# Kernel optimization log

Measured on AMD Instinct MI355X. Metric: run time of the kernel, lower is better.

## Reference

```python
import jax, jax.numpy as jnp
import numpy as np

D = 64       # link_state_dim
RU = 256     # readout_units
N = 50000    # num_edges (total links)
E = 800000   # number of (main, neighbour) message pairs
K_PATHS = 8
T_STEPS = 3


def setup_inputs() -> dict:
    key = jax.random.key(0)
    ks = jax.random.split(key, 10)
    std = 0.1  # init_weight uses normal(std=0.1) for Linear/GRUCell weights
    return {
        'links_state': jax.random.normal(ks[0], (N, D), dtype=jnp.float32),
        'id_mainEdges': jax.random.randint(ks[1], (E,), 0, N),
        'id_neighbourEdges': jax.random.randint(ks[2], (E,), 0, N),
        'W_msg': std * jax.random.normal(ks[3], (D, 2 * D), dtype=jnp.float32),
        'b_msg': jnp.zeros((D,), jnp.float32),
        'W_ih': std * jax.random.normal(ks[4], (3 * D, D), dtype=jnp.float32),
        'W_hh': std * jax.random.normal(ks[5], (3 * D, D), dtype=jnp.float32),
        'b_ih': jnp.zeros((3 * D,), jnp.float32),
        'b_hh': jnp.zeros((3 * D,), jnp.float32),
        'Wr1': std * jax.random.normal(ks[6], (RU, D), dtype=jnp.float32),
        'br1': jnp.zeros((RU,), jnp.float32),
        'Wr2': std * jax.random.normal(ks[7], (RU, RU), dtype=jnp.float32),
        'br2': jnp.zeros((RU,), jnp.float32),
        'Wr3': std * jax.random.normal(ks[8], (1, RU), dtype=jnp.float32),
        'br3': jnp.zeros((1,), jnp.float32),
        'K': K_PATHS,
        'T': T_STEPS,
        'num_edges': N,
    }


def _gru_cell(x, h, W_ih, W_hh, b_ih, b_hh):
    gi = x @ W_ih.T + b_ih            # [N, 3D]
    gh = h @ W_hh.T + b_hh            # [N, 3D]
    i_r, i_z, i_n = jnp.split(gi, 3, axis=1)
    h_r, h_z, h_n = jnp.split(gh, 3, axis=1)
    r = jax.nn.sigmoid(i_r + h_r)
    z = jax.nn.sigmoid(i_z + h_z)
    n = jnp.tanh(i_n + r * h_n)
    return (1.0 - z) * n + z * h


def reference(links_state, id_mainEdges, id_neighbourEdges, W_msg, b_msg,
              W_ih, W_hh, b_ih, b_hh, Wr1, br1, Wr2, br2, Wr3, br3,
              K, T, num_edges):
    for _ in range(T):  # fixed small message-passing depth
        # gather + concat: [E, 2D]
        cat = jnp.concatenate([links_state[id_mainEdges],
                               links_state[id_neighbourEdges]], axis=1)
        m = jax.nn.selu(cat @ W_msg.T + b_msg)                       # [E, D]
        links_M = jax.ops.segment_sum(m, id_neighbourEdges,
                                      num_segments=num_edges)        # [N, D]
        links_state = _gru_cell(links_M, links_state, W_ih, W_hh, b_ih, b_hh)
    # group edges into K paths (contiguous blocks, per K_paths_ids construction)
    per_path = num_edges // K
    path_ids = jnp.arange(num_edges) // per_path
    k_path_outputs = jax.ops.segment_sum(links_state, path_ids,
                                         num_segments=K)             # [K, D]
    h = jax.nn.selu(k_path_outputs @ Wr1.T + br1)
    h = jax.nn.selu(h @ Wr2.T + br2)
    logits = (h @ Wr3.T + br3).reshape(-1)                           # [K]
    return jax.nn.softmax(logits)  # Categorical probs over K paths
```

## Files before the change

### kernel.cpp

```cpp
#include <hip/hip_runtime.h>
#include <hip/hip_bf16.h>

#define D 64
#define CAP 5120

typedef _Float16 f16;
typedef _Float16 f16x2 __attribute__((ext_vector_type(2)));
typedef _Float16 f16x4 __attribute__((ext_vector_type(4)));
typedef _Float16 f16x8 __attribute__((ext_vector_type(8)));
typedef float f32x16 __attribute__((ext_vector_type(16)));

#define MFMA_F16(a, b, c) __builtin_amdgcn_mfma_f32_32x32x16_f16(a, b, c, 0, 0, 0)

__device__ __forceinline__ float selu_f(float x) {
    const float SC = 1.0507009873554805f;
    const float AL = 1.6732632423543772f;
    return x > 0.f ? SC * x : SC * AL * (__expf(x) - 1.f);
}
__device__ __forceinline__ float sigmoid_f(float x) { return 1.f / (1.f + __expf(-x)); }
__device__ __forceinline__ float tanh_f(float x) {
    float s = x < 0.f ? -1.f : 1.f;
    float t = __expf(-2.f * fabsf(x));
    return s * (1.f - t) / (1.f + t);
}
__device__ __forceinline__ float dot4(float4 a, float4 b, float acc) {
    acc = fmaf(a.x, b.x, acc);
    acc = fmaf(a.y, b.y, acc);
    acc = fmaf(a.z, b.z, acc);
    return fmaf(a.w, b.w, acc);
}
__device__ __forceinline__ f32x16 zero16() {
    f32x16 v;
#pragma unroll
    for (int i = 0; i < 16; ++i) v[i] = 0.f;
    return v;
}

__global__ void __launch_bounds__(256) bucketpack_kernel(
    const int* __restrict__ idm, const int* __restrict__ idn,
    int* __restrict__ cursor, uint2* __restrict__ barr,
    const float* __restrict__ Wih, const float* __restrict__ Whh,
    const float* __restrict__ Wmsg, f16* __restrict__ w16,
    float* __restrict__ kp, int* __restrict__ rdcnt,
    int E, int NBK, int NBB) {
    __shared__ int hist[256];
    __shared__ int gbase[256];
    __shared__ int loff[256];
    int t = threadIdx.x;
    if ((int)blockIdx.x >= NBB) {
        int idx = ((int)blockIdx.x - NBB) * 256 + t;
        if (idx < 512) kp[idx] = 0.f;
        if (idx == 0) *rdcnt = 0;
        int g = idx >> 12;
        int rem = idx & 4095;
        int d = rem >> 6, k0 = rem & 63;
        float v;
        if (g < 3)      v = Wih[(g * 64 + d) * 64 + k0];
        else if (g < 6) v = Whh[((g - 3) * 64 + d) * 64 + k0];
        else            v = Wmsg[d * 128 + (g - 6) * 64 + k0];
        w16[g * 4096 + d * 64 + (k0 ^ ((d & 7) << 3))] = (f16)v;
        return;
    }
    if (t < NBK) hist[t] = 0;
    __syncthreads();
    int tile = blockIdx.x * 2048;
    int n_[8], m_[8], b_[8];
#pragma unroll
    for (int j = 0; j < 8; ++j) {
        int e = tile + j * 256 + t;
        if (e < E) {
            n_[j] = idn[e];
            m_[j] = idm[e];
            b_[j] = n_[j] >> 8;
            atomicAdd(&hist[b_[j]], 1);
        } else {
            b_[j] = -1;
        }
    }
    __syncthreads();
    if (t < NBK) {
        gbase[t] = hist[t] ? atomicAdd(&cursor[t], hist[t]) : 0;
        loff[t] = 0;
    }
    __syncthreads();
#pragma unroll
    for (int j = 0; j < 8; ++j) {
        if (b_[j] >= 0) {
            int r = atomicAdd(&loff[b_[j]], 1);
            uint2 e;
            e.x = (unsigned)n_[j];
            e.y = (unsigned)m_[j];
            barr[(size_t)b_[j] * CAP + gbase[b_[j]] + r] = e;
        }
    }
}

__global__ void __launch_bounds__(256) csryz0_kernel(
    const uint2* __restrict__ barr, const int* __restrict__ cursor,
    int* __restrict__ row_start, int* __restrict__ csr_src,
    const float* __restrict__ x, const f16* __restrict__ w16,
    f16* __restrict__ y16, f16* __restrict__ z16,
    int N, int E, int NT, int NBK, int YZGRID) {
    __shared__ int hist[256];
    __shared__ int offs[256];
    __shared__ int curc[256];
    __shared__ int red[256];
    __shared__ int ldsIdm[CAP];
    __shared__ int baseSh;
    __shared__ __align__(16) f16 wlds[2 * 4096];
    __shared__ __align__(16) f16 xh[64 * 64];
    int t = threadIdx.x;
    if ((int)blockIdx.x < NBK) {
        int b = blockIdx.x;
        int cntb = cursor[b];
        red[t] = (t < b) ? cursor[t] : 0;
        __syncthreads();
        for (int off = 128; off > 0; off >>= 1) {
            if (t < off) red[t] += red[t + off];
            __syncthreads();
        }
        if (t == 0) baseSh = red[0];
        hist[t] = 0;
        __syncthreads();
        int base = baseSh;
        for (int i = t; i < cntb; i += 256) {
            int n = (int)(barr[(size_t)b * CAP + i].x) & 255;
            atomicAdd(&hist[n], 1);
        }
        __syncthreads();
        int v0 = hist[t];
        offs[t] = v0;
        __syncthreads();
        for (int off = 1; off < 256; off <<= 1) {
            int v = offs[t];
            int u = (t >= off) ? offs[t - off] : 0;
            __syncthreads();
            offs[t] = v + u;
            __syncthreads();
        }
        int excl = offs[t] - v0;
        curc[t] = excl;
        int node = (b << 8) + t;
        if (node < N) row_start[node] = base + excl;
        if (b == NBK - 1 && t == 0) row_start[N] = E;
        __syncthreads();
        for (int i = t; i < cntb; i += 256) {
            uint2 e = barr[(size_t)b * CAP + i];
            int r = atomicAdd(&curc[e.x & 255], 1);
            ldsIdm[r] = (int)e.y;
        }
        __syncthreads();
        for (int i = t; i < cntb; i += 256) csr_src[base + i] = ldsIdm[i];
        return;
    }
    int yb = (int)blockIdx.x - NBK;
#pragma unroll
    for (int it = 0; it < 4; ++it) {
        int idx = (it * 256 + t) * 8;
        *(f16x8*)&wlds[idx] = *(const f16x8*)&w16[6 * 4096 + idx];
    }
    int lane = t & 63;
    int w = t >> 6;
    int ng = w >> 1;
    int dh = w & 1;
    int arow = ng * 32 + (lane & 31);
    int arow64 = arow * 64;
    int axor = (arow & 7) << 3;
    int bcol = dh * 32 + (lane & 31);
    int bxor = (bcol & 7) << 3;
    int kg = (lane >> 5) * 8;
    __syncthreads();
    for (int tile = yb; tile < NT; tile += YZGRID) {
        int base = tile * 64;
#pragma unroll
        for (int it = 0; it < 4; ++it) {
            int idx = it * 256 + t;
            int node = idx >> 4, k0 = (idx & 15) * 4;
            int gn = base + node;
            f16x4 v;
            if (gn < N) {
                float4 f4 = *(const float4*)&x[(size_t)gn * 64 + k0];
                v[0] = (f16)f4.x; v[1] = (f16)f4.y; v[2] = (f16)f4.z; v[3] = (f16)f4.w;
            } else {
#pragma unroll
                for (int u = 0; u < 4; ++u) v[u] = (f16)0.f;
            }
            *(f16x4*)&xh[node * 64 + (k0 ^ ((node & 7) << 3))] = v;
        }
        __syncthreads();
        f32x16 aY = zero16(), aZ = zero16();
#pragma unroll
        for (int ks = 0; ks < 4; ++ks) {
            int kb = ks * 16 + kg;
            f16x8 ah = *(const f16x8*)&xh[arow64 + (kb ^ axor)];
            int wof = bcol * 64 + (kb ^ bxor);
            aY = MFMA_F16(ah, *(const f16x8*)&wlds[0 * 4096 + wof], aY);
            aZ = MFMA_F16(ah, *(const f16x8*)&wlds[1 * 4096 + wof], aZ);
        }
#pragma unroll
        for (int r = 0; r < 16; ++r) {
            int rowC = (r & 3) + 8 * (r >> 2) + 4 * (lane >> 5);
            int gn = base + ng * 32 + rowC;
            if (gn < N) {
                size_t o = (size_t)gn * 64 + bcol;
                y16[o] = (f16)aY[r];
                z16[o] = (f16)aZ[r];
            }
        }
        __syncthreads();
    }
}

__global__ void __launch_bounds__(256) gather_kernel(
    const f16* __restrict__ y16, const f16* __restrict__ z16,
    const float* __restrict__ bmsg, const int* __restrict__ row_start,
    const int* __restrict__ csr_src, f16* __restrict__ M16, int N) {
    int lane = threadIdx.x & 63;
    int sub = lane >> 5;
    int d0 = (lane & 31) * 2;
    int wave = blockIdx.x * (blockDim.x >> 6) + (threadIdx.x >> 6);
    int nwaves = gridDim.x * (blockDim.x >> 6);
    float b0 = bmsg[d0], b1 = bmsg[d0 + 1];
    for (int i = wave; i < N; i += nwaves) {
        f16x2 zv = *(const f16x2*)&z16[(size_t)i * 64 + d0];
        float zb0 = (float)zv[0] + b0;
        float zb1 = (float)zv[1] + b1;
        int s1 = row_start[i + 1];
        float m0 = 0.f, m1 = 0.f;
        int s = row_start[i] + sub;
        for (; s + 6 < s1; s += 8) {
            int e0 = csr_src[s],     e1 = csr_src[s + 2];
            int e2 = csr_src[s + 4], e3 = csr_src[s + 6];
            f16x2 v0 = *(const f16x2*)&y16[(size_t)e0 * 64 + d0];
            f16x2 v1 = *(const f16x2*)&y16[(size_t)e1 * 64 + d0];
            f16x2 v2 = *(const f16x2*)&y16[(size_t)e2 * 64 + d0];
            f16x2 v3 = *(const f16x2*)&y16[(size_t)e3 * 64 + d0];
            m0 += selu_f((float)v0[0] + zb0);
            m1 += selu_f((float)v0[1] + zb1);
            m0 += selu_f((float)v1[0] + zb0);
            m1 += selu_f((float)v1[1] + zb1);
            m0 += selu_f((float)v2[0] + zb0);
            m1 += selu_f((float)v2[1] + zb1);
            m0 += selu_f((float)v3[0] + zb0);
            m1 += selu_f((float)v3[1] + zb1);
        }
        for (; s < s1; s += 2) {
            int e0 = csr_src[s];
            f16x2 v0 = *(const f16x2*)&y16[(size_t)e0 * 64 + d0];
            m0 += selu_f((float)v0[0] + zb0);
            m1 += selu_f((float)v0[1] + zb1);
        }
        m0 += __shfl_xor(m0, 32, 64);
        m1 += __shfl_xor(m1, 32, 64);
        if (sub == 0) {
            f16x2 mv; mv[0] = (f16)m0; mv[1] = (f16)m1;
            *(f16x2*)&M16[(size_t)i * 64 + d0] = mv;
        }
    }
}

__global__ void __launch_bounds__(256, 2) gruyz_kernel(
    const f16* __restrict__ M16, const float* __restrict__ hin,
    float* __restrict__ hout,
    const float* __restrict__ bih, const float* __restrict__ bhh,
    const f16* __restrict__ w16, f16* __restrict__ y16, f16* __restrict__ z16,
    float* __restrict__ kp, int N, int NT, int PER, int doYZ) {
    __shared__ __align__(16) f16 wlds[8 * 4096];
    __shared__ __align__(16) f16 xm[64 * 64];
    __shared__ __align__(16) f16 xh[64 * 64];
    int t = threadIdx.x;
#pragma unroll 4
    for (int it = 0; it < 16; ++it) {
        int idx = (it * 256 + t) * 8;
        *(f16x8*)&wlds[idx] = *(const f16x8*)&w16[idx];
    }
    int lane = t & 63;
    int w = t >> 6;
    int ng = w >> 1;
    int dh = w & 1;
    int arow = ng * 32 + (lane & 31);
    int arow64 = arow * 64;
    int axor = (arow & 7) << 3;
    int bcol = dh * 32 + (lane & 31);
    int bxor = (bcol & 7) << 3;
    int kg = (lane >> 5) * 8;
    float bIR = bih[bcol], bIZ = bih[64 + bcol], bIN = bih[128 + bcol];
    float bHR = bhh[bcol], bHZ = bhh[64 + bcol], bHN = bhh[128 + bcol];
    float* pathbuf = (float*)xm;
    __syncthreads();
    for (int tile = blockIdx.x; tile < NT; tile += gridDim.x) {
        int base = tile * 64;
#pragma unroll
        for (int it = 0; it < 2; ++it) {
            int idx = it * 256 + t;
            int node = idx >> 3, k0 = (idx & 7) * 8;
            int gn = base + node;
            f16x8 v;
            if (gn < N) v = *(const f16x8*)&M16[(size_t)gn * 64 + k0];
            else {
#pragma unroll
                for (int u = 0; u < 8; ++u) v[u] = (f16)0.f;
            }
            *(f16x8*)&xm[node * 64 + (k0 ^ ((node & 7) << 3))] = v;
        }
#pragma unroll
        for (int it = 0; it < 4; ++it) {
            int idx = it * 256 + t;
            int node = idx >> 4, k0 = (idx & 15) * 4;
            int gn = base + node;
            f16x4 v;
            if (gn < N) {
                float4 f4 = *(const float4*)&hin[(size_t)gn * 64 + k0];
                v[0] = (f16)f4.x; v[1] = (f16)f4.y; v[2] = (f16)f4.z; v[3] = (f16)f4.w;
            } else {
#pragma unroll
                for (int u = 0; u < 4; ++u) v[u] = (f16)0.f;
            }
            *(f16x4*)&xh[node * 64 + (k0 ^ ((node & 7) << 3))] = v;
        }
        __syncthreads();

        f32x16 aIR = zero16(), aIZ = zero16(), aIN = zero16();
        f32x16 aHR = zero16(), aHZ = zero16(), aHN = zero16();
#pragma unroll
        for (int ks = 0; ks < 4; ++ks) {
            int kb = ks * 16 + kg;
            f16x8 am = *(const f16x8*)&xm[arow64 + (kb ^ axor)];
            f16x8 ah = *(const f16x8*)&xh[arow64 + (kb ^ axor)];
            int wof = bcol * 64 + (kb ^ bxor);
            aIR = MFMA_F16(am, *(const f16x8*)&wlds[0 * 4096 + wof], aIR);
            aIZ = MFMA_F16(am, *(const f16x8*)&wlds[1 * 4096 + wof], aIZ);
            aIN = MFMA_F16(am, *(const f16x8*)&wlds[2 * 4096 + wof], aIN);
            aHR = MFMA_F16(ah, *(const f16x8*)&wlds[3 * 4096 + wof], aHR);
            aHZ = MFMA_F16(ah, *(const f16x8*)&wlds[4 * 4096 + wof], aHZ);
            aHN = MFMA_F16(ah, *(const f16x8*)&wlds[5 * 4096 + wof], aHN);
        }
        __syncthreads();

        int pbase = base / PER;
        int boundary = (pbase + 1) * PER;
        if (!doYZ) {
            if (t < 128) pathbuf[t] = 0.f;
            __syncthreads();
        }
#pragma unroll
        for (int r = 0; r < 16; ++r) {
            int rowC = (r & 3) + 8 * (r >> 2) + 4 * (lane >> 5);
            int nodeLocal = ng * 32 + rowC;
            int gn = base + nodeLocal;
            float hnew = 0.f;
            bool valid = gn < N;
            if (valid) {
                size_t o = (size_t)gn * 64 + bcol;
                float hold = hin[o];
                float rr = sigmoid_f(aIR[r] + bIR + aHR[r] + bHR);
                float zz = sigmoid_f(aIZ[r] + bIZ + aHZ[r] + bHZ);
                float nn = tanh_f(aIN[r] + bIN + rr * (aHN[r] + bHN));
                hnew = (1.f - zz) * nn + zz * hold;
                hout[o] = hnew;
            }
            if (doYZ) {
                xm[nodeLocal * 64 + (bcol ^ ((rowC & 7) << 3))] = (f16)hnew;
            } else if (valid) {
                int pidx = (gn >= boundary) ? 1 : 0;
                atomicAdd(&pathbuf[pidx * 64 + bcol], hnew);
            }
        }
        if (doYZ) {
            __syncthreads();
            f32x16 aY = zero16(), aZ = zero16();
#pragma unroll
            for (int ks = 0; ks < 4; ++ks) {
                int kb = ks * 16 + kg;
                f16x8 ahn2 = *(const f16x8*)&xm[arow64 + (kb ^ axor)];
                int wof = bcol * 64 + (kb ^ bxor);
                aY = MFMA_F16(ahn2, *(const f16x8*)&wlds[6 * 4096 + wof], aY);
                aZ = MFMA_F16(ahn2, *(const f16x8*)&wlds[7 * 4096 + wof], aZ);
            }
#pragma unroll
            for (int r = 0; r < 16; ++r) {
                int rowC = (r & 3) + 8 * (r >> 2) + 4 * (lane >> 5);
                int gn = base + ng * 32 + rowC;
                if (gn < N) {
                    size_t o = (size_t)gn * 64 + bcol;
                    y16[o] = (f16)aY[r];
                    z16[o] = (f16)aZ[r];
                }
            }
        } else {
            __syncthreads();
            if (t < 128) {
                int p = pbase + (t >> 6);
                float v = pathbuf[t];
                if (p < 8 && v != 0.f) atomicAdd(&kp[p * 64 + (t & 63)], v);
            }
        }
        __syncthreads();
    }
}

__global__ void __launch_bounds__(256) readout_kernel(
    const float* __restrict__ kp, const float* __restrict__ Wr1,
    const float* __restrict__ br1, const float* __restrict__ Wr2,
    const float* __restrict__ br2, const float* __restrict__ Wr3,
    const float* __restrict__ br3, float* __restrict__ lgbuf,
    int* __restrict__ rdcnt, float* __restrict__ out) {
    int p = blockIdx.x;
    int t = threadIdx.x;
    __shared__ __align__(16) float kps[64];
    __shared__ __align__(16) float h1[256];
    __shared__ float red[256];
    if (t < 64) kps[t] = kp[p * 64 + t];
    __syncthreads();
    float acc = br1[t];
#pragma unroll
    for (int d4 = 0; d4 < 16; ++d4) {
        float4 wv = *(const float4*)&Wr1[t * 64 + d4 * 4];
        float4 kv = *(const float4*)&kps[d4 * 4];
        acc = dot4(wv, kv, acc);
    }
    h1[t] = selu_f(acc);
    __syncthreads();
    float acc2 = br2[t];
#pragma unroll 8
    for (int j4 = 0; j4 < 64; ++j4) {
        float4 wv = *(const float4*)&Wr2[t * 256 + j4 * 4];
        float4 hv = *(const float4*)&h1[j4 * 4];
        acc2 = dot4(wv, hv, acc2);
    }
    float h2v = selu_f(acc2);
    red[t] = Wr3[t] * h2v;
    __syncthreads();
    for (int off = 128; off > 0; off >>= 1) {
        if (t < off) red[t] += red[t + off];
        __syncthreads();
    }
    if (t == 0) {
        float logit = red[0] + br3[0];
        atomicExch(&lgbuf[p], logit);
        __threadfence();
        int old = atomicAdd(rdcnt, 1);
        if (old == 7) {
            float lg[8];
#pragma unroll
            for (int j = 0; j < 8; ++j) lg[j] = atomicAdd(&lgbuf[j], 0.f);
            float mx = lg[0];
            for (int j = 1; j < 8; ++j) mx = fmaxf(mx, lg[j]);
            float s = 0.f, e[8];
            for (int j = 0; j < 8; ++j) {
                e[j] = __expf(lg[j] - mx);
                s += e[j];
            }
            for (int j = 0; j < 8; ++j) out[j] = e[j] / s;
        }
    }
}

extern "C" void kernel_launch(void* const* d_in, const int* in_sizes, int n_in,
                              void* d_out, int out_size, void* d_ws, size_t ws_size,
                              hipStream_t stream) {
    const float* links_state = (const float*)d_in[0];
    const int* idm = (const int*)d_in[1];
    const int* idn = (const int*)d_in[2];
    const float* Wmsg = (const float*)d_in[3];
    const float* bmsg = (const float*)d_in[4];
    const float* Wih = (const float*)d_in[5];
    const float* Whh = (const float*)d_in[6];
    const float* bih = (const float*)d_in[7];
    const float* bhh = (const float*)d_in[8];
    const float* Wr1 = (const float*)d_in[9];
    const float* br1 = (const float*)d_in[10];
    const float* Wr2 = (const float*)d_in[11];
    const float* br2 = (const float*)d_in[12];
    const float* Wr3 = (const float*)d_in[13];
    const float* br3 = (const float*)d_in[14];

    const int N = in_sizes[0] / D;
    const int E = in_sizes[1];
    const int K = 8, T = 3;
    const int NBK = (N + 255) >> 8;
    const int NBB = (E + 2047) / 2048;
    const int NT = (N + 63) / 64;
    const int PER = N / K;

    float* ws = (float*)d_ws;
    size_t nd = (size_t)N * D;
    float* cur = ws;
    f16* y16 = (f16*)(ws + nd);
    f16* z16 = y16 + nd;
    f16* M16 = z16 + nd;
    float* kp = (float*)(M16 + nd);
    float* lgbuf = kp + 512;
    int* rdcnt = (int*)(lgbuf + 8);
    f16* w16 = (f16*)(rdcnt + 8);
    uint2* barr = (uint2*)(w16 + 32768);
    int* ibase = (int*)(barr + (size_t)NBK * CAP);
    int* cursor = ibase;
    int* row_start = ibase + 256;
    int* csr_src = row_start + N + 1;

    hipMemsetAsync(cursor, 0, 256 * sizeof(int), stream);
    bucketpack_kernel<<<dim3(NBB + 128), dim3(256), 0, stream>>>(
        idm, idn, cursor, barr, Wih, Whh, Wmsg, w16, kp, rdcnt, E, NBK, NBB);
    csryz0_kernel<<<dim3(NBK + 512), dim3(256), 0, stream>>>(
        barr, cursor, row_start, csr_src, links_state, w16, y16, z16, N, E, NT, NBK, 512);

    for (int t = 0; t < T; ++t) {
        gather_kernel<<<dim3(2048), dim3(256), 0, stream>>>(y16, z16, bmsg, row_start,
                                                            csr_src, M16, N);
        gruyz_kernel<<<dim3(512), dim3(256), 0, stream>>>(
            M16, (t == 0) ? links_state : cur, cur, bih, bhh, w16, y16, z16, kp, N, NT, PER,
            t < T - 1 ? 1 : 0);
    }

    readout_kernel<<<dim3(8), dim3(256), 0, stream>>>(kp, Wr1, br1, Wr2, br2, Wr3, br3,
                                                      lgbuf, rdcnt, (float*)d_out);
}
```

Before: 215.5 us.

## Store gathered message projection in fp8 and pack bucket entries into 32 bits

The per-neighbour projection y, which is gathered once per edge in every message-passing step, is now stored as fp8 (e4m3) instead of fp16, halving the bytes read by the random gather. Bucket entries are packed into a single 32-bit word (main index shifted left by 8, low byte of the neighbour index), halving the bucket-sort traffic. The fp8 rounding of y adds quantisation error to the messages that is summed over about 16 neighbours per node and carried through three GRU steps, so accuracy tolerance is a risk. The packing assumes main-edge indices fit in 24 bits.

```diff
diff --git a/kernel.cpp b/kernel.cpp
--- a/kernel.cpp
+++ b/kernel.cpp
@@ -35,10 +35,13 @@
     for (int i = 0; i < 16; ++i) v[i] = 0.f;
     return v;
 }
+__device__ __forceinline__ unsigned char to_fp8(float v) {
+    return (unsigned char)(__builtin_amdgcn_cvt_pk_fp8_f32(v, v, 0, false) & 0xff);
+}
 
 __global__ void __launch_bounds__(256) bucketpack_kernel(
     const int* __restrict__ idm, const int* __restrict__ idn,
-    int* __restrict__ cursor, uint2* __restrict__ barr,
+    int* __restrict__ cursor, unsigned* __restrict__ barr,
     const float* __restrict__ Wih, const float* __restrict__ Whh,
     const float* __restrict__ Wmsg, f16* __restrict__ w16,
     float* __restrict__ kp, int* __restrict__ rdcnt,
@@ -87,19 +90,17 @@
     for (int j = 0; j < 8; ++j) {
         if (b_[j] >= 0) {
             int r = atomicAdd(&loff[b_[j]], 1);
-            uint2 e;
-            e.x = (unsigned)n_[j];
-            e.y = (unsigned)m_[j];
-            barr[(size_t)b_[j] * CAP + gbase[b_[j]] + r] = e;
+            barr[(size_t)b_[j] * CAP + gbase[b_[j]] + r] =
+                ((unsigned)m_[j] << 8) | ((unsigned)n_[j] & 255u);
         }
     }
 }
 
 __global__ void __launch_bounds__(256) csryz0_kernel(
-    const uint2* __restrict__ barr, const int* __restrict__ cursor,
+    const unsigned* __restrict__ barr, const int* __restrict__ cursor,
     int* __restrict__ row_start, int* __restrict__ csr_src,
     const float* __restrict__ x, const f16* __restrict__ w16,
-    f16* __restrict__ y16, f16* __restrict__ z16,
+    unsigned char* __restrict__ y8, f16* __restrict__ z16,
     int N, int E, int NT, int NBK, int YZGRID) {
     __shared__ int hist[256];
     __shared__ int offs[256];
@@ -124,7 +125,7 @@
         __syncthreads();
         int base = baseSh;
         for (int i = t; i < cntb; i += 256) {
-            int n = (int)(barr[(size_t)b * CAP + i].x) & 255;
+            int n = (int)(barr[(size_t)b * CAP + i] & 255u);
             atomicAdd(&hist[n], 1);
         }
         __syncthreads();
@@ -145,9 +146,9 @@
         if (b == NBK - 1 && t == 0) row_start[N] = E;
         __syncthreads();
         for (int i = t; i < cntb; i += 256) {
-            uint2 e = barr[(size_t)b * CAP + i];
-            int r = atomicAdd(&curc[e.x & 255], 1);
-            ldsIdm[r] = (int)e.y;
+            unsigned e = barr[(size_t)b * CAP + i];
+            int r = atomicAdd(&curc[e & 255u], 1);
+            ldsIdm[r] = (int)(e >> 8);
         }
         __syncthreads();
         for (int i = t; i < cntb; i += 256) csr_src[base + i] = ldsIdm[i];
@@ -203,7 +204,7 @@
             int gn = base + ng * 32 + rowC;
             if (gn < N) {
                 size_t o = (size_t)gn * 64 + bcol;
-                y16[o] = (f16)aY[r];
+                y8[o] = to_fp8(aY[r]);
                 z16[o] = (f16)aZ[r];
             }
         }
@@ -212,7 +213,7 @@
 }
 
 __global__ void __launch_bounds__(256) gather_kernel(
-    const f16* __restrict__ y16, const f16* __restrict__ z16,
+    const unsigned char* __restrict__ y8, const f16* __restrict__ z16,
     const float* __restrict__ bmsg, const int* __restrict__ row_start,
     const int* __restrict__ csr_src, f16* __restrict__ M16, int N) {
     int lane = threadIdx.x & 63;
@@ -231,24 +232,24 @@
         for (; s + 6 < s1; s += 8) {
             int e0 = csr_src[s],     e1 = csr_src[s + 2];
             int e2 = csr_src[s + 4], e3 = csr_src[s + 6];
-            f16x2 v0 = *(const f16x2*)&y16[(size_t)e0 * 64 + d0];
-            f16x2 v1 = *(const f16x2*)&y16[(size_t)e1 * 64 + d0];
-            f16x2 v2 = *(const f16x2*)&y16[(size_t)e2 * 64 + d0];
-            f16x2 v3 = *(const f16x2*)&y16[(size_t)e3 * 64 + d0];
-            m0 += selu_f((float)v0[0] + zb0);
-            m1 += selu_f((float)v0[1] + zb1);
-            m0 += selu_f((float)v1[0] + zb0);
-            m1 += selu_f((float)v1[1] + zb1);
-            m0 += selu_f((float)v2[0] + zb0);
-            m1 += selu_f((float)v2[1] + zb1);
-            m0 += selu_f((float)v3[0] + zb0);
-            m1 += selu_f((float)v3[1] + zb1);
+            int v0 = *(const unsigned short*)&y8[(size_t)e0 * 64 + d0];
+            int v1 = *(const unsigned short*)&y8[(size_t)e1 * 64 + d0];
+            int v2 = *(const unsigned short*)&y8[(size_t)e2 * 64 + d0];
+            int v3 = *(const unsigned short*)&y8[(size_t)e3 * 64 + d0];
+            m0 += selu_f(__builtin_amdgcn_cvt_f32_fp8(v0, 0) + zb0);
+            m1 += selu_f(__builtin_amdgcn_cvt_f32_fp8(v0, 1) + zb1);
+            m0 += selu_f(__builtin_amdgcn_cvt_f32_fp8(v1, 0) + zb0);
+            m1 += selu_f(__builtin_amdgcn_cvt_f32_fp8(v1, 1) + zb1);
+            m0 += selu_f(__builtin_amdgcn_cvt_f32_fp8(v2, 0) + zb0);
+            m1 += selu_f(__builtin_amdgcn_cvt_f32_fp8(v2, 1) + zb1);
+            m0 += selu_f(__builtin_amdgcn_cvt_f32_fp8(v3, 0) + zb0);
+            m1 += selu_f(__builtin_amdgcn_cvt_f32_fp8(v3, 1) + zb1);
         }
         for (; s < s1; s += 2) {
             int e0 = csr_src[s];
-            f16x2 v0 = *(const f16x2*)&y16[(size_t)e0 * 64 + d0];
-            m0 += selu_f((float)v0[0] + zb0);
-            m1 += selu_f((float)v0[1] + zb1);
+            int v0 = *(const unsigned short*)&y8[(size_t)e0 * 64 + d0];
+            m0 += selu_f(__builtin_amdgcn_cvt_f32_fp8(v0, 0) + zb0);
+            m1 += selu_f(__builtin_amdgcn_cvt_f32_fp8(v0, 1) + zb1);
         }
         m0 += __shfl_xor(m0, 32, 64);
         m1 += __shfl_xor(m1, 32, 64);
@@ -263,7 +264,8 @@
     const f16* __restrict__ M16, const float* __restrict__ hin,
     float* __restrict__ hout,
     const float* __restrict__ bih, const float* __restrict__ bhh,
-    const f16* __restrict__ w16, f16* __restrict__ y16, f16* __restrict__ z16,
+    const f16* __restrict__ w16, unsigned char* __restrict__ y8,
+    f16* __restrict__ z16,
     float* __restrict__ kp, int N, int NT, int PER, int doYZ) {
     __shared__ __align__(16) f16 wlds[8 * 4096];
     __shared__ __align__(16) f16 xm[64 * 64];
@@ -383,7 +385,7 @@
                 int gn = base + ng * 32 + rowC;
                 if (gn < N) {
                     size_t o = (size_t)gn * 64 + bcol;
-                    y16[o] = (f16)aY[r];
+                    y8[o] = to_fp8(aY[r]);
                     z16[o] = (f16)aZ[r];
                 }
             }
@@ -486,14 +488,14 @@
     float* ws = (float*)d_ws;
     size_t nd = (size_t)N * D;
     float* cur = ws;
-    f16* y16 = (f16*)(ws + nd);
-    f16* z16 = y16 + nd;
+    f16* z16 = (f16*)(ws + nd);
     f16* M16 = z16 + nd;
-    float* kp = (float*)(M16 + nd);
+    unsigned char* y8 = (unsigned char*)(M16 + nd);
+    float* kp = (float*)(y8 + nd);
     float* lgbuf = kp + 512;
     int* rdcnt = (int*)(lgbuf + 8);
     f16* w16 = (f16*)(rdcnt + 8);
-    uint2* barr = (uint2*)(w16 + 32768);
+    unsigned* barr = (unsigned*)(w16 + 32768);
     int* ibase = (int*)(barr + (size_t)NBK * CAP);
     int* cursor = ibase;
     int* row_start = ibase + 256;
@@ -503,13 +505,13 @@
     bucketpack_kernel<<<dim3(NBB + 128), dim3(256), 0, stream>>>(
         idm, idn, cursor, barr, Wih, Whh, Wmsg, w16, kp, rdcnt, E, NBK, NBB);
     csryz0_kernel<<<dim3(NBK + 512), dim3(256), 0, stream>>>(
-        barr, cursor, row_start, csr_src, links_state, w16, y16, z16, N, E, NT, NBK, 512);
+        barr, cursor, row_start, csr_src, links_state, w16, y8, z16, N, E, NT, NBK, 512);
 
     for (int t = 0; t < T; ++t) {
-        gather_kernel<<<dim3(2048), dim3(256), 0, stream>>>(y16, z16, bmsg, row_start,
+        gather_kernel<<<dim3(2048), dim3(256), 0, stream>>>(y8, z16, bmsg, row_start,
                                                             csr_src, M16, N);
         gruyz_kernel<<<dim3(512), dim3(256), 0, stream>>>(
-            M16, (t == 0) ? links_state : cur, cur, bih, bhh, w16, y16, z16, kp, N, NT, PER,
+            M16, (t == 0) ? links_state : cur, cur, bih, bhh, w16, y8, z16, kp, N, NT, PER,
             t < T - 1 ? 1 : 0);
     }
 
```

Result: no change. 211.8 us (-1.7%).
